# Optimization experiments

Measured on AMD Instinct MI355X. Metric: run time of the kernel, lower is better.

The kernel has to match this reference:

```python
import jax, jax.numpy as jnp
import numpy as np

N = 100_000      # nodes
E = 3_200_000    # edges (avg degree 32)
F_IN, H1, H2, C = 1433, 200, 80, 7


def setup_inputs() -> dict:
    key = jax.random.key(0)
    ks = jax.random.split(key, 10)
    x = jax.random.normal(ks[0], (N, F_IN), jnp.float32)
    edge_src = jax.random.randint(ks[1], (E,), 0, N)
    edge_dst = jax.random.randint(ks[2], (E,), 0, N)
    edge_w = jax.random.uniform(ks[3], (E,), jnp.float32)
    # GraphConvolution.reset_parameters: uniform(-1/sqrt(out), 1/sqrt(out))
    s1 = 1.0 / np.sqrt(H1).astype(np.float32)
    W1 = jax.random.uniform(ks[4], (F_IN, H1), jnp.float32, -s1, s1)
    b1 = jax.random.uniform(ks[5], (H1,), jnp.float32, -s1, s1)
    s2 = 1.0 / np.sqrt(H2).astype(np.float32)
    W2 = jax.random.uniform(ks[6], (H1, H2), jnp.float32, -s2, s2)
    b2 = jax.random.uniform(ks[7], (H2,), jnp.float32, -s2, s2)
    # nn.Linear(80, 7)
    sf = 1.0 / np.sqrt(H2).astype(np.float32)
    Wfc = jax.random.uniform(ks[8], (H2, C), jnp.float32, -sf, sf)
    bfc = jax.random.uniform(ks[9], (C,), jnp.float32, -sf, sf)
    return {"x": x, "edge_src": edge_src, "edge_dst": edge_dst, "edge_w": edge_w,
            "W1": W1, "b1": b1, "W2": W2, "b2": b2, "Wfc": Wfc, "bfc": bfc}


def reference(x, edge_src, edge_dst, edge_w, W1, b1, W2, b2, Wfc, bfc):
    n = x.shape[0]

    def spmm(h):  # out[dst] += w * h[src]  == torch.spmm(adj, h)
        return jax.ops.segment_sum(edge_w[:, None] * h[edge_src], edge_dst,
                                   num_segments=n)

    h = jax.nn.relu(spmm(x @ W1) + b1)   # GraphConvolution 1 + ReLU (dropout: eval)
    h = jax.nn.relu(spmm(h @ W2) + b2)   # GraphConvolution 2 + ReLU
    return h @ Wfc + bfc                  # fc_1: [N, 7] logits
```

## Files before the change

### kernel.cpp

```cpp
#include <hip/hip_runtime.h>

#define F_IN 1433
#define H1 200
#define H2 80
#define NC 7

typedef __bf16 bf16x8 __attribute__((ext_vector_type(8)));
typedef float f32x4 __attribute__((ext_vector_type(4)));

__device__ __forceinline__ unsigned short bf16_bits(__bf16 h) {
    union { __bf16 h; unsigned short u; } c; c.h = h; return c.u;
}
__device__ __forceinline__ void split_bf16(float a, __bf16& hi, __bf16& lo) {
    hi = (__bf16)a;
    lo = (__bf16)(a - (float)hi);
}

struct AF { float v[8]; };

__device__ __forceinline__ void glds16(const void* g, void* l) {
    __builtin_amdgcn_global_load_lds(
        (const __attribute__((address_space(1))) unsigned int*)g,
        (__attribute__((address_space(3))) unsigned int*)l, 16, 0, 0);
}

template <int K, int KSTEPS, int COLS, int WR, int WC, int MT, int NT, bool BIAS>
__global__ __launch_bounds__(512, 4)
void gemm_mfma_bstage(const float* __restrict__ A, const unsigned short* __restrict__ Bpre,
                      const float* __restrict__ bias, float* __restrict__ C,
                      int M, int NREAL) {
    static_assert(WR * WC == 8, "8 waves");
    static_assert(WR * MT * 16 == 128, "rows");
    static_assert(WC * NT * 16 == COLS, "cols");
    constexpr int THREADS = 512;
    constexpr int PER_STEP = 2 * 4 * COLS * 8;
    constexpr int CH = COLS * 8;
    constexpr bool PART = (KSTEPS * 32 > K);

    __shared__ alignas(16) unsigned short Bs[PER_STEP];

    const int tid = threadIdx.x;
    const int wave = tid >> 6, lane = tid & 63;
    const int l15 = lane & 15, l4 = lane >> 4;
    const int wr = wave / WC, wc = wave % WC;
    const int row0 = blockIdx.x * 128 + wr * (MT * 16);
    const int colbase = wc * (NT * 16);

    f32x4 acc[MT][NT];
    #pragma unroll
    for (int m = 0; m < MT; ++m)
        #pragma unroll
        for (int n = 0; n < NT; ++n) acc[m][n] = (f32x4){0.f, 0.f, 0.f, 0.f};

    const float* arow[MT];
    #pragma unroll
    for (int m = 0; m < MT; ++m) {
        int r = row0 + m * 16 + l15;
        if (r >= M) r = M - 1;
        arow[m] = A + (size_t)r * K;
    }

    auto loadA = [&](int s, AF* dst) {
        const int kb = s * 32 + l4 * 8;
        #pragma unroll
        for (int m = 0; m < MT; ++m) {
            const float* ap = arow[m] + kb;
            if (PART && s == KSTEPS - 1) {
                #pragma unroll
                for (int j = 0; j < 8; ++j) dst[m].v[j] = (kb + j < K) ? ap[j] : 0.f;
            } else {
                #pragma unroll
                for (int j = 0; j < 8; ++j) dst[m].v[j] = ap[j];
            }
        }
    };

    auto stageB = [&](int s) {
        const unsigned short* src = Bpre + (size_t)s * PER_STEP;
        #pragma unroll 4
        for (int c = tid; c < CH; c += THREADS)
            glds16(src + (size_t)c * 8, &Bs[c * 8]);
    };

    AF aCur[MT], aNxt[MT];
    loadA(0, aCur);
    stageB(0);

    for (int s = 0; s < KSTEPS; ++s) {
        __syncthreads();
        bf16x8 aHi[MT], aLo[MT];
        #pragma unroll
        for (int m = 0; m < MT; ++m)
            #pragma unroll
            for (int j = 0; j < 8; ++j) {
                __bf16 hi, lo;
                split_bf16(aCur[m].v[j], hi, lo);
                aHi[m][j] = hi;
                aLo[m][j] = lo;
            }
        if (s + 1 < KSTEPS) loadA(s + 1, aNxt);

        #pragma unroll
        for (int n = 0; n < NT; ++n) {
            const int colb = colbase + n * 16 + l15;
            bf16x8 bHi = *(const bf16x8*)&Bs[((0 + l4) * COLS + colb) * 8];
            bf16x8 bLo = *(const bf16x8*)&Bs[((4 + l4) * COLS + colb) * 8];
            #pragma unroll
            for (int m = 0; m < MT; ++m) {
                acc[m][n] = __builtin_amdgcn_mfma_f32_16x16x32_bf16(aHi[m], bHi, acc[m][n], 0, 0, 0);
                acc[m][n] = __builtin_amdgcn_mfma_f32_16x16x32_bf16(aLo[m], bHi, acc[m][n], 0, 0, 0);
                acc[m][n] = __builtin_amdgcn_mfma_f32_16x16x32_bf16(aHi[m], bLo, acc[m][n], 0, 0, 0);
            }
        }
        __syncthreads();
        if (s + 1 < KSTEPS) stageB(s + 1);
        #pragma unroll
        for (int m = 0; m < MT; ++m) aCur[m] = aNxt[m];
    }

    #pragma unroll
    for (int m = 0; m < MT; ++m) {
        const int rbase = row0 + m * 16 + l4 * 4;
        #pragma unroll
        for (int n = 0; n < NT; ++n) {
            int col = colbase + n * 16 + l15;
            if (col >= NREAL) continue;
            float bv = BIAS ? bias[col] : 0.f;
            #pragma unroll
            for (int r = 0; r < 4; ++r) {
                int gr = rbase + r;
                if (gr < M) C[(size_t)gr * NREAL + col] = acc[m][n][r] + bv;
            }
        }
    }
}

__global__ void convert_B(const float* __restrict__ W, unsigned short* __restrict__ out,
                          int K, int NREAL, int KSTEPS, int COLS) {
    const int per = 2 * 4 * COLS * 8;
    long long total = (long long)KSTEPS * per;
    long long i = (long long)blockIdx.x * blockDim.x + threadIdx.x;
    long long stride = (long long)gridDim.x * blockDim.x;
    for (; i < total; i += stride) {
        int s = (int)(i / per);
        int r = (int)(i % per);
        int hl = r / (4 * COLS * 8); r %= 4 * COLS * 8;
        int k8 = r / (COLS * 8);     r %= COLS * 8;
        int col = r >> 3, j = r & 7;
        int k = s * 32 + k8 * 8 + j;
        float v = (k < K && col < NREAL) ? W[(size_t)k * NREAL + col] : 0.f;
        __bf16 hi, lo;
        split_bf16(v, hi, lo);
        out[i] = bf16_bits(hl ? lo : hi);
    }
}

__global__ void gemm_tiled(const float* __restrict__ A, const float* __restrict__ B,
                           const float* __restrict__ bias, float* __restrict__ C,
                           int M, int K, int N, int tilesN) {
    const int bx = blockIdx.x % tilesN;
    const int by = blockIdx.x / tilesN;
    const int tid = threadIdx.x;
    const int tx = tid & 15, ty = tid >> 4;
    __shared__ float Asf[64][17];
    __shared__ float Bsf[16][65];
    float acc[4][4] = {};
    const int row0 = by * 64, col0 = bx * 64;
    for (int k0 = 0; k0 < K; k0 += 16) {
        #pragma unroll
        for (int l = 0; l < 4; ++l) {
            int e = tid + l * 256;
            int r = e >> 4, kk = e & 15;
            int gr = row0 + r, gk = k0 + kk;
            Asf[r][kk] = (gr < M && gk < K) ? A[(size_t)gr * K + gk] : 0.f;
        }
        #pragma unroll
        for (int l = 0; l < 4; ++l) {
            int e = tid + l * 256;
            int kk = e >> 6, c = e & 63;
            int gk = k0 + kk, gc = col0 + c;
            Bsf[kk][c] = (gk < K && gc < N) ? B[(size_t)gk * N + gc] : 0.f;
        }
        __syncthreads();
        #pragma unroll
        for (int kk = 0; kk < 16; ++kk) {
            float a[4], b[4];
            #pragma unroll
            for (int i = 0; i < 4; ++i) a[i] = Asf[ty + 16 * i][kk];
            #pragma unroll
            for (int j = 0; j < 4; ++j) b[j] = Bsf[kk][tx + 16 * j];
            #pragma unroll
            for (int i = 0; i < 4; ++i)
                #pragma unroll
                for (int j = 0; j < 4; ++j) acc[i][j] += a[i] * b[j];
        }
        __syncthreads();
    }
    #pragma unroll
    for (int i = 0; i < 4; ++i) {
        int gr = row0 + ty + 16 * i;
        if (gr >= M) continue;
        #pragma unroll
        for (int j = 0; j < 4; ++j) {
            int gc = col0 + tx + 16 * j;
            if (gc >= N) continue;
            float v = acc[i][j];
            if (bias) v += bias[gc];
            C[(size_t)gr * N + gc] = v;
        }
    }
}

__global__ void zero_ints(int* __restrict__ p, int n) {
    int i = blockIdx.x * blockDim.x + threadIdx.x;
    int stride = gridDim.x * blockDim.x;
    for (; i < n; i += stride) p[i] = 0;
}

__global__ void hist_dst(const int* __restrict__ dst, int* __restrict__ counts, int E) {
    int i = blockIdx.x * blockDim.x + threadIdx.x;
    int stride = gridDim.x * blockDim.x;
    for (; i < E; i += stride) atomicAdd(&counts[dst[i]], 1);
}

__global__ void chunk_sums(const int* __restrict__ counts, int* __restrict__ csum, int N) {
    __shared__ int s[256];
    int b = blockIdx.x, t = threadIdx.x;
    int base = b * 2048 + t * 8;
    int loc = 0;
    #pragma unroll
    for (int i = 0; i < 8; ++i) {
        int gi = base + i;
        if (gi < N) loc += counts[gi];
    }
    s[t] = loc;
    __syncthreads();
    for (int off = 128; off > 0; off >>= 1) {
        if (t < off) s[t] += s[t + off];
        __syncthreads();
    }
    if (t == 0) csum[b] = s[0];
}

__global__ void scan_chunks(const int* __restrict__ csum, int* __restrict__ cbase, int NB) {
    if (blockIdx.x == 0 && threadIdx.x == 0) {
        int run = 0;
        for (int b = 0; b < NB; ++b) { cbase[b] = run; run += csum[b]; }
    }
}

__global__ void scan_final(const int* __restrict__ counts, const int* __restrict__ cbase,
                           int* __restrict__ row_start, int* __restrict__ cursor, int N) {
    __shared__ int s[256];
    int b = blockIdx.x, t = threadIdx.x;
    int base = b * 2048 + t * 8;
    int loc = 0;
    #pragma unroll
    for (int i = 0; i < 8; ++i) {
        int gi = base + i;
        if (gi < N) loc += counts[gi];
    }
    s[t] = loc;
    __syncthreads();
    for (int off = 1; off < 256; off <<= 1) {
        int v = (t >= off) ? s[t - off] : 0;
        __syncthreads();
        s[t] += v;
        __syncthreads();
    }
    int run = cbase[b] + s[t] - loc;
    for (int i = 0; i < 8; ++i) {
        int gi = base + i;
        if (gi < N) {
            row_start[gi] = run;
            cursor[gi] = run;
            run += counts[gi];
        }
    }
}

__global__ void scatter_edges(const int* __restrict__ src, const int* __restrict__ dst,
                              const float* __restrict__ w, int* __restrict__ cursor,
                              int2* __restrict__ csr, int E) {
    int i = blockIdx.x * blockDim.x + threadIdx.x;
    int stride = gridDim.x * blockDim.x;
    for (; i < E; i += stride) {
        int d = dst[i];
        int pos = atomicAdd(&cursor[d], 1);
        csr[pos] = make_int2(src[i], __float_as_int(w[i]));
    }
}

template <int D, bool RELU>
__global__ __launch_bounds__(256)
void spmm_csr(const float* __restrict__ h, const int2* __restrict__ csr,
              const int* __restrict__ row_start, const int* __restrict__ counts,
              const float* __restrict__ bias, float* __restrict__ out, int N) {
    constexpr int VF = D / 4;
    constexpr int G = 256 / VF;
    const int g = threadIdx.x / VF;
    const int slot = threadIdx.x - g * VF;
    if (g >= G) return;
    const int row = blockIdx.x * G + g;
    if (row >= N) return;

    const int p = row_start[row], len = counts[row];
    f32x4 acc = ((const f32x4*)bias)[slot];

    int2 e0 = make_int2(0, 0), e1 = e0, e2 = e0, e3 = e0;
    if (len > 0) e0 = csr[p];
    if (len > 1) e1 = csr[p + 1];
    if (len > 2) e2 = csr[p + 2];
    if (len > 3) e3 = csr[p + 3];

    for (int q = 0; q < len; q += 4) {
        const int2 c0 = e0, c1 = e1, c2 = e2, c3 = e3;
        const int rem = len - q;
        if (q + 4 < len) e0 = csr[p + q + 4];
        if (q + 5 < len) e1 = csr[p + q + 5];
        if (q + 6 < len) e2 = csr[p + q + 6];
        if (q + 7 < len) e3 = csr[p + q + 7];
        f32x4 h0 = ((const f32x4*)(h + (size_t)c0.x * D))[slot];
        acc += h0 * __int_as_float(c0.y);
        if (rem > 1) {
            f32x4 h1 = ((const f32x4*)(h + (size_t)c1.x * D))[slot];
            acc += h1 * __int_as_float(c1.y);
        }
        if (rem > 2) {
            f32x4 h2 = ((const f32x4*)(h + (size_t)c2.x * D))[slot];
            acc += h2 * __int_as_float(c2.y);
        }
        if (rem > 3) {
            f32x4 h3 = ((const f32x4*)(h + (size_t)c3.x * D))[slot];
            acc += h3 * __int_as_float(c3.y);
        }
    }
    if (RELU) {
        #pragma unroll
        for (int c = 0; c < 4; ++c) acc[c] = acc[c] > 0.f ? acc[c] : 0.f;
    }
    ((f32x4*)(out + (size_t)row * D))[slot] = acc;
}

__global__ void init_bias_kernel(float* __restrict__ agg, const float* __restrict__ bias,
                                 long long n, int D) {
    long long i = (long long)blockIdx.x * blockDim.x + threadIdx.x;
    long long stride = (long long)gridDim.x * blockDim.x;
    for (; i < n; i += stride) agg[i] = bias[(int)(i % D)];
}

template <int D>
__global__ void spmm_edges(const float* __restrict__ h, const int* __restrict__ src,
                           const int* __restrict__ dst, const float* __restrict__ w,
                           float* __restrict__ agg, int E) {
    int e = blockIdx.x * 4 + (threadIdx.x >> 6);
    int lane = threadIdx.x & 63;
    if (e >= E) return;
    int s = src[e], d = dst[e];
    float wt = w[e];
    const float* hs = h + (size_t)s * D;
    float* ad = agg + (size_t)d * D;
    for (int j = lane; j < D; j += 64) atomicAdd(&ad[j], wt * hs[j]);
}

__global__ void relu_kernel(float* __restrict__ x, long long n) {
    long long i = (long long)blockIdx.x * blockDim.x + threadIdx.x;
    long long stride = (long long)gridDim.x * blockDim.x;
    for (; i < n; i += stride) {
        float v = x[i];
        x[i] = v > 0.f ? v : 0.f;
    }
}

extern "C" void kernel_launch(void* const* d_in, const int* in_sizes, int n_in,
                              void* d_out, int out_size, void* d_ws, size_t ws_size,
                              hipStream_t stream) {
    const float* x        = (const float*)d_in[0];
    const int*   edge_src = (const int*)d_in[1];
    const int*   edge_dst = (const int*)d_in[2];
    const float* edge_w   = (const float*)d_in[3];
    const float* W1       = (const float*)d_in[4];
    const float* b1       = (const float*)d_in[5];
    const float* W2       = (const float*)d_in[6];
    const float* b2       = (const float*)d_in[7];
    const float* Wfc      = (const float*)d_in[8];
    const float* bfc      = (const float*)d_in[9];
    float* out = (float*)d_out;

    const int N = in_sizes[0] / F_IN;
    const int E = in_sizes[1];
    const int NB = (N + 2047) / 2048;

    float* h0  = (float*)d_ws;
    float* agg = h0 + (size_t)N * H1;
    int* counts    = (int*)(agg + (size_t)N * H1);
    int* row_start = counts + N;
    int* cursor    = row_start + N;
    int* csum      = cursor + N;
    int* cbase     = csum + NB;
    size_t csr_off = (size_t)(cbase + NB) - (size_t)d_ws;
    csr_off = (csr_off + 15) & ~(size_t)15;
    int2* csr = (int2*)((char*)d_ws + csr_off);
    size_t boff = csr_off + (size_t)E * sizeof(int2);
    boff = (boff + 15) & ~(size_t)15;
    const size_t B1n = 45ull * 2 * 4 * 224 * 8;
    const size_t B2n = 7ull * 2 * 4 * 80 * 8;
    const size_t Bfn = 3ull * 2 * 4 * 16 * 8;
    unsigned short* B1p = (unsigned short*)((char*)d_ws + boff);
    unsigned short* B2p = B1p + B1n;
    unsigned short* Bfp = B2p + B2n;
    size_t needed = boff + (B1n + B2n + Bfn) * sizeof(unsigned short);

    float* h1 = agg;
    float* h2 = h0;
    float* h3 = agg;

    const int MB = (N + 127) / 128;

    if (ws_size >= needed) {
        convert_B<<<(int)((B1n + 255) / 256), 256, 0, stream>>>(W1, B1p, F_IN, H1, 45, 224);
        convert_B<<<(int)((B2n + 255) / 256), 256, 0, stream>>>(W2, B2p, H1, H2, 7, 80);
        convert_B<<<(int)((Bfn + 255) / 256), 256, 0, stream>>>(Wfc, Bfp, H2, NC, 3, 16);

        zero_ints<<<256, 256, 0, stream>>>(counts, N);
        hist_dst<<<2048, 256, 0, stream>>>(edge_dst, counts, E);
        chunk_sums<<<NB, 256, 0, stream>>>(counts, csum, N);
        scan_chunks<<<1, 64, 0, stream>>>(csum, cbase, NB);
        scan_final<<<NB, 256, 0, stream>>>(counts, cbase, row_start, cursor, N);
        scatter_edges<<<2048, 256, 0, stream>>>(edge_src, edge_dst, edge_w, cursor, csr, E);

        gemm_mfma_bstage<F_IN, 45, 224, 4, 2, 2, 7, false><<<MB, 512, 0, stream>>>(x, B1p, nullptr, h0, N, H1);
        {
            constexpr int G1 = 256 / (H1 / 4);
            spmm_csr<H1, true><<<(N + G1 - 1) / G1, 256, 0, stream>>>(h0, csr, row_start, counts, b1, h1, N);
        }

        gemm_mfma_bstage<H1, 7, 80, 8, 1, 1, 5, false><<<MB, 512, 0, stream>>>(h1, B2p, nullptr, h2, N, H2);
        {
            constexpr int G2 = 256 / (H2 / 4);
            spmm_csr<H2, true><<<(N + G2 - 1) / G2, 256, 0, stream>>>(h2, csr, row_start, counts, b2, h3, N);
        }

        gemm_mfma_bstage<H2, 3, 16, 8, 1, 1, 1, true><<<MB, 512, 0, stream>>>(h3, Bfp, bfc, out, N, NC);
    } else {
        const int tilesM = (N + 63) / 64;
        gemm_tiled<<<tilesM * 4, 256, 0, stream>>>(x, W1, nullptr, h0, N, F_IN, H1, 4);
        init_bias_kernel<<<2048, 256, 0, stream>>>(agg, b1, (long long)N * H1, H1);
        spmm_edges<H1><<<(E + 3) / 4, 256, 0, stream>>>(h0, edge_src, edge_dst, edge_w, agg, E);
        relu_kernel<<<2048, 256, 0, stream>>>(agg, (long long)N * H1);
        gemm_tiled<<<tilesM * 2, 256, 0, stream>>>(h1, W2, nullptr, h2, N, H1, H2, 2);
        init_bias_kernel<<<2048, 256, 0, stream>>>(agg, b2, (long long)N * H2, H2);
        spmm_edges<H2><<<(E + 3) / 4, 256, 0, stream>>>(h2, edge_src, edge_dst, edge_w, agg, E);
        relu_kernel<<<2048, 256, 0, stream>>>(agg, (long long)N * H2);
        gemm_tiled<<<tilesM, 256, 0, stream>>>(h3, Wfc, bfc, out, N, H2, NC, 1);
    }
}
```

Baseline: 1.243 ms.

## Fuse final linear layer into second SpMM and halve GEMM block size

The final fc layer (80->7) is now computed inside the second SpMM kernel: each block aggregates its rows into shared memory, applies ReLU, then multiplies by Wfc held in shared memory. This removes the write and re-read of the N x 80 intermediate, a separate GEMM launch and the Wfc conversion. Separately, the MFMA GEMM tile shrinks from 128 rows and 8 waves to 64 rows and 4 waves, doubling the grid. That gives more blocks for load balance and occupancy, but each B tile staged in shared memory is reused across fewer rows.

```diff
diff --git a/kernel.cpp b/kernel.cpp
--- a/kernel.cpp
+++ b/kernel.cpp
@@ -25,14 +25,14 @@
 }
 
 template <int K, int KSTEPS, int COLS, int WR, int WC, int MT, int NT, bool BIAS>
-__global__ __launch_bounds__(512, 4)
+__global__ __launch_bounds__(256, 4)
 void gemm_mfma_bstage(const float* __restrict__ A, const unsigned short* __restrict__ Bpre,
                       const float* __restrict__ bias, float* __restrict__ C,
                       int M, int NREAL) {
-    static_assert(WR * WC == 8, "8 waves");
-    static_assert(WR * MT * 16 == 128, "rows");
+    static_assert(WR * WC == 4, "4 waves");
+    static_assert(WR * MT * 16 == 64, "rows");
     static_assert(WC * NT * 16 == COLS, "cols");
-    constexpr int THREADS = 512;
+    constexpr int THREADS = 256;
     constexpr int PER_STEP = 2 * 4 * COLS * 8;
     constexpr int CH = COLS * 8;
     constexpr bool PART = (KSTEPS * 32 > K);
@@ -43,7 +43,7 @@
     const int wave = tid >> 6, lane = tid & 63;
     const int l15 = lane & 15, l4 = lane >> 4;
     const int wr = wave / WC, wc = wave % WC;
-    const int row0 = blockIdx.x * 128 + wr * (MT * 16);
+    const int row0 = blockIdx.x * 64 + wr * (MT * 16);
     const int colbase = wc * (NT * 16);
 
     f32x4 acc[MT][NT];
@@ -342,6 +342,74 @@
     ((f32x4*)(out + (size_t)row * D))[slot] = acc;
 }
 
+template <int D, int NCOL>
+__global__ __launch_bounds__(256)
+void spmm_fc(const float* __restrict__ h, const int2* __restrict__ csr,
+             const int* __restrict__ row_start, const int* __restrict__ counts,
+             const float* __restrict__ bias, const float* __restrict__ Wfc,
+             const float* __restrict__ bfc, float* __restrict__ out, int N) {
+    constexpr int VF = D / 4;
+    constexpr int G = 256 / VF;
+    __shared__ float sh[G][D];
+    __shared__ float sW[D * NCOL];
+    __shared__ float sb[NCOL];
+    for (int i = threadIdx.x; i < D * NCOL; i += 256) sW[i] = Wfc[i];
+    if (threadIdx.x < NCOL) sb[threadIdx.x] = bfc[threadIdx.x];
+
+    const int g = threadIdx.x / VF;
+    const int slot = threadIdx.x - g * VF;
+    const int row = blockIdx.x * G + g;
+    const bool active = (g < G) && (row < N);
+
+    if (active) {
+        const int p = row_start[row], len = counts[row];
+        f32x4 acc = ((const f32x4*)bias)[slot];
+        int2 e0 = make_int2(0, 0), e1 = e0, e2 = e0, e3 = e0;
+        if (len > 0) e0 = csr[p];
+        if (len > 1) e1 = csr[p + 1];
+        if (len > 2) e2 = csr[p + 2];
+        if (len > 3) e3 = csr[p + 3];
+        for (int q = 0; q < len; q += 4) {
+            const int2 c0 = e0, c1 = e1, c2 = e2, c3 = e3;
+            const int rem = len - q;
+            if (q + 4 < len) e0 = csr[p + q + 4];
+            if (q + 5 < len) e1 = csr[p + q + 5];
+            if (q + 6 < len) e2 = csr[p + q + 6];
+            if (q + 7 < len) e3 = csr[p + q + 7];
+            f32x4 h0 = ((const f32x4*)(h + (size_t)c0.x * D))[slot];
+            acc += h0 * __int_as_float(c0.y);
+            if (rem > 1) {
+                f32x4 h1 = ((const f32x4*)(h + (size_t)c1.x * D))[slot];
+                acc += h1 * __int_as_float(c1.y);
+            }
+            if (rem > 2) {
+                f32x4 h2 = ((const f32x4*)(h + (size_t)c2.x * D))[slot];
+                acc += h2 * __int_as_float(c2.y);
+            }
+            if (rem > 3) {
+                f32x4 h3 = ((const f32x4*)(h + (size_t)c3.x * D))[slot];
+                acc += h3 * __int_as_float(c3.y);
+            }
+        }
+        #pragma unroll
+        for (int c = 0; c < 4; ++c) acc[c] = acc[c] > 0.f ? acc[c] : 0.f;
+        ((f32x4*)&sh[g][0])[slot] = acc;
+    }
+    __syncthreads();
+
+    const int idx = threadIdx.x;
+    if (idx < G * NCOL) {
+        const int gr = idx / NCOL, c = idx - gr * NCOL;
+        const int orow = blockIdx.x * G + gr;
+        if (orow < N) {
+            float s = sb[c];
+            #pragma unroll 8
+            for (int j = 0; j < D; ++j) s += sh[gr][j] * sW[j * NCOL + c];
+            out[(size_t)orow * NCOL + c] = s;
+        }
+    }
+}
+
 __global__ void init_bias_kernel(float* __restrict__ agg, const float* __restrict__ bias,
                                  long long n, int D) {
     long long i = (long long)blockIdx.x * blockDim.x + threadIdx.x;
@@ -405,22 +473,18 @@
     boff = (boff + 15) & ~(size_t)15;
     const size_t B1n = 45ull * 2 * 4 * 224 * 8;
     const size_t B2n = 7ull * 2 * 4 * 80 * 8;
-    const size_t Bfn = 3ull * 2 * 4 * 16 * 8;
     unsigned short* B1p = (unsigned short*)((char*)d_ws + boff);
     unsigned short* B2p = B1p + B1n;
-    unsigned short* Bfp = B2p + B2n;
-    size_t needed = boff + (B1n + B2n + Bfn) * sizeof(unsigned short);
+    size_t needed = boff + (B1n + B2n) * sizeof(unsigned short);
 
     float* h1 = agg;
     float* h2 = h0;
-    float* h3 = agg;
-
-    const int MB = (N + 127) / 128;
+
+    const int MB = (N + 63) / 64;
 
     if (ws_size >= needed) {
         convert_B<<<(int)((B1n + 255) / 256), 256, 0, stream>>>(W1, B1p, F_IN, H1, 45, 224);
         convert_B<<<(int)((B2n + 255) / 256), 256, 0, stream>>>(W2, B2p, H1, H2, 7, 80);
-        convert_B<<<(int)((Bfn + 255) / 256), 256, 0, stream>>>(Wfc, Bfp, H2, NC, 3, 16);
 
         zero_ints<<<256, 256, 0, stream>>>(counts, N);
         hist_dst<<<2048, 256, 0, stream>>>(edge_dst, counts, E);
@@ -429,19 +493,18 @@
         scan_final<<<NB, 256, 0, stream>>>(counts, cbase, row_start, cursor, N);
         scatter_edges<<<2048, 256, 0, stream>>>(edge_src, edge_dst, edge_w, cursor, csr, E);
 
-        gemm_mfma_bstage<F_IN, 45, 224, 4, 2, 2, 7, false><<<MB, 512, 0, stream>>>(x, B1p, nullptr, h0, N, H1);
+        gemm_mfma_bstage<F_IN, 45, 224, 2, 2, 2, 7, false><<<MB, 256, 0, stream>>>(x, B1p, nullptr, h0, N, H1);
         {
             constexpr int G1 = 256 / (H1 / 4);
             spmm_csr<H1, true><<<(N + G1 - 1) / G1, 256, 0, stream>>>(h0, csr, row_start, counts, b1, h1, N);
         }
 
-        gemm_mfma_bstage<H1, 7, 80, 8, 1, 1, 5, false><<<MB, 512, 0, stream>>>(h1, B2p, nullptr, h2, N, H2);
+        gemm_mfma_bstage<H1, 7, 80, 4, 1, 1, 5, false><<<MB, 256, 0, stream>>>(h1, B2p, nullptr, h2, N, H2);
+
         {
             constexpr int G2 = 256 / (H2 / 4);
-            spmm_csr<H2, true><<<(N + G2 - 1) / G2, 256, 0, stream>>>(h2, csr, row_start, counts, b2, h3, N);
-        }
-
-        gemm_mfma_bstage<H2, 3, 16, 8, 1, 1, 1, true><<<MB, 512, 0, stream>>>(h3, Bfp, bfc, out, N, NC);
+            spmm_fc<H2, NC><<<(N + G2 - 1) / G2, 256, 0, stream>>>(h2, csr, row_start, counts, b2, Wfc, bfc, out, N);
+        }
     } else {
         const int tilesM = (N + 63) / 64;
         gemm_tiled<<<tilesM * 4, 256, 0, stream>>>(x, W1, nullptr, h0, N, F_IN, H1, 4);
@@ -452,6 +515,6 @@
         init_bias_kernel<<<2048, 256, 0, stream>>>(agg, b2, (long long)N * H2, H2);
         spmm_edges<H2><<<(E + 3) / 4, 256, 0, stream>>>(h2, edge_src, edge_dst, edge_w, agg, E);
         relu_kernel<<<2048, 256, 0, stream>>>(agg, (long long)N * H2);
-        gemm_tiled<<<tilesM, 256, 0, stream>>>(h3, Wfc, bfc, out, N, H2, NC, 1);
-    }
-}
+        gemm_tiled<<<tilesM, 256, 0, stream>>>(agg, Wfc, bfc, out, N, H2, NC, 1);
+    }
+}
```

After: 1.266 ms. About the same (+1.9%).
